# Kernel tuning notes

Hardware: AMD Instinct MI355X
Metric: run time of the kernel (lower is better)

## Reference

```python
import jax, jax.numpy as jnp
import numpy as np
import math

B, S, D, H, L, F = 32, 512, 512, 8, 4, 1024
TD = 4 * D  # time embedding dim
DH = D // H
SCALE = 1.0 / math.sqrt(DH)


def _ln(x, g, b):
    m = jnp.mean(x, -1, keepdims=True)
    v = jnp.var(x, -1, keepdims=True)
    return (x - m) * jax.lax.rsqrt(v + 1e-5) * g + b


def setup_inputs() -> dict:
    key = jax.random.key(0)
    ks = jax.random.split(key, 12)
    w = lambda k, shp: jax.random.normal(k, shp, dtype=jnp.float32) * 0.02
    return {
        "x": jax.random.normal(ks[0], (B, S, D), dtype=jnp.float32),
        "time": jax.random.uniform(ks[1], (B,), dtype=jnp.float32) * 1000.0,
        "time_w1": w(ks[2], (TD, D)), "time_b1": jnp.zeros((TD,), jnp.float32),
        "time_w2": w(ks[3], (TD, TD)), "time_b2": jnp.zeros((TD,), jnp.float32),
        "Wq": w(ks[4], (L, D, D)), "bq": jnp.zeros((L, D), jnp.float32),
        "Wk": w(ks[5], (L, D, D)), "bk": jnp.zeros((L, D), jnp.float32),
        "Wv": w(ks[6], (L, D, D)), "bv": jnp.zeros((L, D), jnp.float32),
        "Wo": w(ks[7], (L, D, D)), "bo": jnp.zeros((L, D), jnp.float32),
        "attn_g": jnp.ones((L, D), jnp.float32), "attn_b": jnp.zeros((L, D), jnp.float32),
        "ffn_g": jnp.ones((L, D), jnp.float32), "ffn_b": jnp.zeros((L, D), jnp.float32),
        "W1": w(ks[8], (L, 2 * F, D)), "b1": jnp.zeros((L, 2 * F), jnp.float32),
        "W2": w(ks[9], (L, D, F)), "b2": jnp.zeros((L, D), jnp.float32),
        "Wt": w(ks[10], (L, 4 * F, TD)), "bt": jnp.zeros((L, 4 * F), jnp.float32),
        "head_g": jnp.ones((D,), jnp.float32), "head_b": jnp.zeros((D,), jnp.float32),
        "Wh": w(ks[11], (D, D)), "bh": jnp.zeros((D,), jnp.float32),
    }


def _forward(x, time, time_w1, time_b1, time_w2, time_b2,
             Wq, bq, Wk, bk, Wv, bv, Wo, bo,
             attn_g, attn_b, ffn_g, ffn_b,
             W1, b1, W2, b2, Wt, bt,
             head_g, head_b, Wh, bh):
    Bsz = x.shape[0]
    # --- sinusoidal time embedding + time MLP ---
    half = D // 2
    freqs = jnp.exp(jnp.arange(half, dtype=jnp.float32) * (-math.log(10000.0) / (half - 1)))
    e = time[:, None] * freqs[None, :]
    temb = jnp.concatenate([jnp.sin(e), jnp.cos(e)], axis=-1)  # [B, D]
    temb = jax.nn.gelu(temb @ time_w1.T + time_b1, approximate=False) @ time_w2.T + time_b2  # [B, 4D]
    for i in range(L):
        # attention (prenorm; block 0 skips the norm since first_prenormalization=False)
        h = x if i == 0 else _ln(x, attn_g[i], attn_b[i])
        q = (h @ Wq[i].T + bq[i]).reshape(Bsz, S, H, DH)
        k = (h @ Wk[i].T + bk[i]).reshape(Bsz, S, H, DH)
        v = (h @ Wv[i].T + bv[i]).reshape(Bsz, S, H, DH)
        logits = jnp.einsum('bqhd,bkhd->bhqk', q, k) * SCALE
        probs = jax.nn.softmax(logits, axis=-1)
        o = jnp.einsum('bhqk,bkhd->bqhd', probs, v).reshape(Bsz, S, D)
        x = x + (o @ Wo[i].T + bo[i])
        # FFN with FiLM time conditioning and ReGLU activation
        h = _ln(x, ffn_g[i], ffn_b[i])
        h1 = h @ W1[i].T + b1[i]  # [B, S, 2F]
        tm = jax.nn.silu(temb) @ Wt[i].T + bt[i]  # [B, 4F]
        scale, shift = jnp.split(tm[:, None, :], 2, axis=-1)  # each [B, 1, 2F]
        h1 = h1 * (scale + 1.0) + shift
        a, g = jnp.split(h1, 2, axis=-1)  # ReGLU: a * relu(g)
        x = x + ((a * jax.nn.relu(g)) @ W2[i].T + b2[i])
    # head: last token -> LayerNorm -> ReLU -> Linear
    z = _ln(x[:, -1], head_g, head_b)
    return jax.nn.relu(z) @ Wh.T + bh


def reference(x, time, time_w1, time_b1, time_w2, time_b2,
              Wq, bq, Wk, bk, Wv, bv, Wo, bo,
              attn_g, attn_b, ffn_g, ffn_b,
              W1, b1, W2, b2, Wt, bt,
              head_g, head_b, Wh, bh):
    return _forward(x, time, time_w1, time_b1, time_w2, time_b2,
                    Wq, bq, Wk, bk, Wv, bv, Wo, bo,
                    attn_g, attn_b, ffn_g, ffn_b,
                    W1, b1, W2, b2, Wt, bt,
                    head_g, head_b, Wh, bh)
```

## Files before the change

### kernel.cpp

```cpp
#include <hip/hip_runtime.h>
#include <math.h>

typedef __bf16 bf16_t;
typedef __bf16 bf16x8 __attribute__((ext_vector_type(8)));
typedef float f32x4 __attribute__((ext_vector_type(4)));

__device__ __forceinline__ void gload_lds16(const void* g, void* l) {
    __builtin_amdgcn_global_load_lds(
        (const __attribute__((address_space(1))) void*)g,
        (__attribute__((address_space(3))) void*)l, 16, 0, 0);
}

__global__ void k_f2b(const float* __restrict__ in, bf16_t* __restrict__ out, int n8) {
    int idx = blockIdx.x * 256 + threadIdx.x;
    if (idx >= n8) return;
    const float* p = in + (size_t)idx * 8;
    bf16x8 r;
#pragma unroll
    for (int j = 0; j < 8; j++) r[j] = (bf16_t)p[j];
    *(bf16x8*)(out + (size_t)idx * 8) = r;
}

__global__ void k_f2b_s(const float* __restrict__ in, bf16_t* __restrict__ out,
                        int seg8, int dstride8) {
    int idx = blockIdx.x * 256 + threadIdx.x;
    int seg = idx / seg8, rem = idx - seg * seg8;
    const float* p = in + (size_t)idx * 8;
    bf16x8 r;
#pragma unroll
    for (int j = 0; j < 8; j++) r[j] = (bf16_t)p[j];
    *(bf16x8*)(out + ((size_t)seg * dstride8 + rem) * 8) = r;
}

__global__ void k_time_embed(const float* __restrict__ time, float* __restrict__ temb0) {
    int b = blockIdx.x;
    int j = threadIdx.x;
    float f = __expf((float)j * -0.036118981458730134f);
    float e = time[b] * f;
    temb0[(size_t)b * 512 + j] = sinf(e);
    temb0[(size_t)b * 512 + 256 + j] = cosf(e);
}

template<bool DO_NORM, bool IN32>
__global__ void k_ln(const void* __restrict__ xp, const float* __restrict__ g,
                     const float* __restrict__ b, bf16_t* __restrict__ out) {
    int row = blockIdx.x * 4 + (threadIdx.x >> 6);
    int lane = threadIdx.x & 63;
    float vals[8];
    if (IN32) {
        const float* xr = (const float*)xp + (size_t)row * 512 + lane * 8;
        float4 v0 = *(const float4*)xr;
        float4 v1 = *(const float4*)(xr + 4);
        vals[0] = v0.x; vals[1] = v0.y; vals[2] = v0.z; vals[3] = v0.w;
        vals[4] = v1.x; vals[5] = v1.y; vals[6] = v1.z; vals[7] = v1.w;
    } else {
        bf16x8 xv = *(const bf16x8*)((const bf16_t*)xp + (size_t)row * 512 + lane * 8);
#pragma unroll
        for (int j = 0; j < 8; j++) vals[j] = (float)xv[j];
    }
    bf16x8 r;
    if (DO_NORM) {
        float s = 0.f, sq = 0.f;
#pragma unroll
        for (int j = 0; j < 8; j++) { s += vals[j]; sq += vals[j] * vals[j]; }
#pragma unroll
        for (int m = 1; m < 64; m <<= 1) { s += __shfl_xor(s, m, 64); sq += __shfl_xor(sq, m, 64); }
        float mean = s * (1.0f / 512.0f);
        float var = sq * (1.0f / 512.0f) - mean * mean;
        float rstd = rsqrtf(var + 1e-5f);
        float4 g0 = *(const float4*)(g + lane * 8);
        float4 g1 = *(const float4*)(g + lane * 8 + 4);
        float4 b0 = *(const float4*)(b + lane * 8);
        float4 b1 = *(const float4*)(b + lane * 8 + 4);
        float gs[8] = {g0.x, g0.y, g0.z, g0.w, g1.x, g1.y, g1.z, g1.w};
        float bs[8] = {b0.x, b0.y, b0.z, b0.w, b1.x, b1.y, b1.z, b1.w};
#pragma unroll
        for (int j = 0; j < 8; j++) r[j] = (bf16_t)((vals[j] - mean) * rstd * gs[j] + bs[j]);
    } else {
#pragma unroll
        for (int j = 0; j < 8; j++) r[j] = (bf16_t)vals[j];
    }
    *(bf16x8*)(out + (size_t)row * 512 + lane * 8) = r;
}

__global__ void k_head_prep(const bf16_t* __restrict__ x, const float* __restrict__ g,
                            const float* __restrict__ b, float* __restrict__ z) {
    int row = blockIdx.x * 4 + (threadIdx.x >> 6);
    int lane = threadIdx.x & 63;
    bf16x8 xv = *(const bf16x8*)(x + ((size_t)row * 512 + 511) * 512 + lane * 8);
    float vals[8];
#pragma unroll
    for (int j = 0; j < 8; j++) vals[j] = (float)xv[j];
    float s = 0.f, sq = 0.f;
#pragma unroll
    for (int j = 0; j < 8; j++) { s += vals[j]; sq += vals[j] * vals[j]; }
#pragma unroll
    for (int m = 1; m < 64; m <<= 1) { s += __shfl_xor(s, m, 64); sq += __shfl_xor(sq, m, 64); }
    float mean = s * (1.0f / 512.0f);
    float var = sq * (1.0f / 512.0f) - mean * mean;
    float rstd = rsqrtf(var + 1e-5f);
    float o[8];
#pragma unroll
    for (int j = 0; j < 8; j++) {
        float gv = g[lane * 8 + j], bv = b[lane * 8 + j];
        o[j] = fmaxf((vals[j] - mean) * rstd * gv + bv, 0.0f);
    }
    float* zr = z + (size_t)row * 512 + lane * 8;
    *(float4*)zr = make_float4(o[0], o[1], o[2], o[3]);
    *(float4*)(zr + 4) = make_float4(o[4], o[5], o[6], o[7]);
}

template<int ACT, int K, bool OUTB>
__global__ __launch_bounds__(256, 2)
void k_gemm_tm(const float* __restrict__ A, const float* __restrict__ W,
               const float* __restrict__ bias, void* __restrict__ outp, int N) {
    __shared__ float Asm[32][516];
    const int t = threadIdx.x;
    const int kq = t & 7, rw = (t >> 3) & 7, bh = t >> 6;
    const int n0 = blockIdx.x * 32;
    float acc[4][8] = {};
    for (int k0 = 0; k0 < K; k0 += 512) {
        __syncthreads();
#pragma unroll
        for (int i = 0; i < 16; i++) {
            int fid = t + i * 256;
            int row = fid >> 7, cc = (fid & 127) << 2;
            *(float4*)&Asm[row][cc] = *(const float4*)&A[(size_t)row * K + k0 + cc];
        }
        __syncthreads();
#pragma unroll 4
        for (int j = 0; j < 16; j++) {
            int kk = kq * 4 + j * 32;
            float4 w4[4];
#pragma unroll
            for (int r = 0; r < 4; r++)
                w4[r] = *(const float4*)&W[(size_t)(n0 + rw + r * 8) * K + k0 + kk];
#pragma unroll
            for (int b = 0; b < 8; b++) {
                float4 a4 = *(const float4*)&Asm[bh * 8 + b][kk];
#pragma unroll
                for (int r = 0; r < 4; r++)
                    acc[r][b] += a4.x * w4[r].x + a4.y * w4[r].y + a4.z * w4[r].z + a4.w * w4[r].w;
            }
        }
    }
#pragma unroll
    for (int m = 1; m < 8; m <<= 1)
#pragma unroll
        for (int r = 0; r < 4; r++)
#pragma unroll
            for (int b = 0; b < 8; b++)
                acc[r][b] += __shfl_xor(acc[r][b], m, 64);
    if (kq == 0) {
#pragma unroll
        for (int r = 0; r < 4; r++) {
            int n = n0 + rw + r * 8;
            float bv = bias[n];
#pragma unroll
            for (int b = 0; b < 8; b++) {
                float v = acc[r][b] + bv;
                if (ACT == 1) v = 0.5f * v * (1.0f + erff(v * 0.70710678118654752f));
                if (ACT == 2) v = v / (1.0f + __expf(-v));
                if (OUTB) ((bf16_t*)outp)[(size_t)(bh * 8 + b) * N + n] = (bf16_t)v;
                else      ((float*)outp)[(size_t)(bh * 8 + b) * N + n] = v;
            }
        }
    }
}

__global__ void k_fill_tmt(const float* __restrict__ bt, float* __restrict__ tm_t) {
    int i = blockIdx.x * 256 + threadIdx.x;
    tm_t[i] = bt[i >> 5];
}

__global__ __launch_bounds__(256, 4)
void k_gemm_wt(const float* __restrict__ Wt, const bf16_t* __restrict__ t2s_b,
               float* __restrict__ tm_t) {
    __shared__ __align__(16) bf16_t Abuf[64 * 64];
    __shared__ __align__(16) bf16_t Bbuf[32 * 64];
    const int tid = threadIdx.x;
    const int m0 = blockIdx.x * 64;
    const int k0 = blockIdx.y * 512;
    const int lane = tid & 63, wave = tid >> 6;
    const int arow = tid >> 2, aseg = tid & 3;
    const int brow = tid >> 3, bseg = tid & 7;
    const int aswz = (arow & 7) << 4;
    const char* Bg = (const char*)t2s_b + (size_t)brow * 4096 + ((bseg * 16) ^ ((brow & 7) << 4));
    char* BbL = (char*)Bbuf + tid * 16;
    const float* Ar0 = Wt + (size_t)(m0 + arow) * 2048 + k0 + aseg * 16;
    f32x4 acc[2] = {};
    for (int kk0 = 0; kk0 < 512; kk0 += 64) {
        float4 a4[4];
#pragma unroll
        for (int i = 0; i < 4; i++) a4[i] = *(const float4*)(Ar0 + kk0 + i * 4);
        __syncthreads();
        gload_lds16(Bg + (size_t)(k0 + kk0) * 2, BbL);
        bf16x8 c0, c1;
#pragma unroll
        for (int i = 0; i < 4; i++) {
            const float* af = (const float*)&a4[i];
#pragma unroll
            for (int j = 0; j < 4; j++) {
                if (i < 2) c0[i * 4 + j] = (bf16_t)af[j];
                else       c1[(i - 2) * 4 + j] = (bf16_t)af[j];
            }
        }
        int base = arow * 128 + aseg * 32;
        *(bf16x8*)((char*)Abuf + (base ^ aswz)) = c0;
        *(bf16x8*)((char*)Abuf + ((base + 16) ^ aswz)) = c1;
        __syncthreads();
#pragma unroll
        for (int kk = 0; kk < 2; kk++) {
            int ar = wave * 16 + (lane & 15);
            bf16x8 af = *(const bf16x8*)((const char*)Abuf + ar * 128 +
                        ((kk * 64 + (lane >> 4) * 16) ^ ((ar & 7) << 4)));
#pragma unroll
            for (int j = 0; j < 2; j++) {
                int br = j * 16 + (lane & 15);
                bf16x8 bfr = *(const bf16x8*)((const char*)Bbuf + br * 128 +
                             ((kk * 64 + (lane >> 4) * 16) ^ ((br & 7) << 4)));
                acc[j] = __builtin_amdgcn_mfma_f32_16x16x32_bf16(af, bfr, acc[j], 0, 0, 0);
            }
        }
    }
#pragma unroll
    for (int j = 0; j < 2; j++)
#pragma unroll
        for (int r = 0; r < 4; r++) {
            int mrow = m0 + wave * 16 + (lane >> 4) * 4 + r;
            atomicAdd(&tm_t[(size_t)mrow * 32 + j * 16 + (lane & 15)], acc[j][r]);
        }
}

enum { EPI_QKV = 0, EPI_RESID = 1, EPI_FILMGLU = 2 };

template<int EPI, int K, int NBY, int BM, bool RS32>
__global__ __launch_bounds__(BM * 2, 4)
void k_gemm_bt(const bf16_t* __restrict__ A, const bf16_t* __restrict__ W,
               const float* __restrict__ bias, const float* __restrict__ bias2,
               const float* __restrict__ bias3,
               void* __restrict__ out0, const void* __restrict__ rsp, void* __restrict__ out2,
               const float* __restrict__ tm) {
    constexpr int T   = BM * 2;
    constexpr int RPR = BM / 4;
    constexpr int BR  = 512 / BM;
    __shared__ __align__(16) bf16_t Abuf[BM * 64];
    __shared__ __align__(16) bf16_t Bbuf[128 * 64];
    const int tid = threadIdx.x;
    const int cpx = gridDim.x >> 3;
    const int wg = (blockIdx.x & 7) * cpx + (blockIdx.x >> 3);
    const int bx = wg / NBY;
    const int by = wg - bx * NBY;
    const int m0 = bx * BM;
    const int lane = tid & 63;
    const int wid = tid >> 6;
    const int wrM = (wid >> 1) * 64;
    const int wN  = wid & 1;
    const int wc  = wN * 64;

    const int srow = tid >> 3;
    const int goff = ((tid & 7) * 16) ^ ((srow & 7) << 4);
    const char* Ag = (const char*)A;
    const char* Wg = (const char*)W;
    char* AbL = (char*)Abuf + tid * 16;
    char* BbL = (char*)Bbuf + tid * 16;
    int growB[BR];
#pragma unroll
    for (int i = 0; i < BR; i++) {
        int r = srow + i * RPR;
        if (EPI == EPI_FILMGLU) {
            int half = (r >> 5) & 1;
            int base = by * 64 + (r >> 6) * 32 + (r & 31);
            growB[i] = half * 1024 + base;
        } else {
            growB[i] = by * 128 + r;
        }
    }

    f32x4 acc[4][4] = {};
    for (int k0 = 0; k0 < K * 2; k0 += 128) {
        __syncthreads();
#pragma unroll
        for (int i = 0; i < 4; i++)
            gload_lds16(Ag + (size_t)(m0 + srow + i * RPR) * (K * 2) + k0 + goff, AbL + i * (T * 16));
#pragma unroll
        for (int i = 0; i < BR; i++)
            gload_lds16(Wg + (size_t)growB[i] * (K * 2) + k0 + goff, BbL + i * (T * 16));
        __syncthreads();
#pragma unroll
        for (int kk = 0; kk < 2; kk++) {
            bf16x8 af[4], bfr[4];
#pragma unroll
            for (int i = 0; i < 4; i++) {
                int ar = wrM + i * 16 + (lane & 15);
                af[i] = *(const bf16x8*)((const char*)Abuf + ar * 128 +
                         ((kk * 64 + (lane >> 4) * 16) ^ ((ar & 7) << 4)));
                int br = wc + i * 16 + (lane & 15);
                bfr[i] = *(const bf16x8*)((const char*)Bbuf + br * 128 +
                         ((kk * 64 + (lane >> 4) * 16) ^ ((br & 7) << 4)));
            }
#pragma unroll
            for (int i = 0; i < 4; i++)
#pragma unroll
                for (int j = 0; j < 4; j++)
                    acc[i][j] = __builtin_amdgcn_mfma_f32_16x16x32_bf16(af[i], bfr[j], acc[i][j], 0, 0, 0);
        }
    }

    const int b = m0 >> 9;
    if (EPI == EPI_QKV) {
        const int which = by >> 2;
        bf16_t* op = (bf16_t*)(which == 0 ? out0 : which == 1 ? (void*)rsp : out2);
        const float* bp = which == 0 ? bias : which == 1 ? bias2 : bias3;
#pragma unroll
        for (int i = 0; i < 4; i++) {
#pragma unroll
            for (int r = 0; r < 4; r++) {
                int s = (m0 + wrM + i * 16 + (lane >> 4) * 4 + r) & 511;
#pragma unroll
                for (int j = 0; j < 4; j++) {
                    int c = (by & 3) * 128 + wc + j * 16 + (lane & 15);
                    float v = acc[i][j][r] + bp[c];
                    int h = c >> 6, dh = c & 63;
                    op[(((size_t)b * 8 + h) * 512 + s) * 64 + dh] = (bf16_t)v;
                }
            }
        }
    } else if (EPI == EPI_RESID) {
        bf16_t* op = (bf16_t*)out0;
#pragma unroll
        for (int i = 0; i < 4; i++) {
#pragma unroll
            for (int r = 0; r < 4; r++) {
                int row = m0 + wrM + i * 16 + (lane >> 4) * 4 + r;
#pragma unroll
                for (int j = 0; j < 4; j++) {
                    int col = by * 128 + wc + j * 16 + (lane & 15);
                    size_t idx = (size_t)row * 512 + col;
                    float rsv = RS32 ? ((const float*)rsp)[idx] : (float)((const bf16_t*)rsp)[idx];
                    op[idx] = (bf16_t)(rsv + acc[i][j][r] + bias[col]);
                }
            }
        }
    } else {
        bf16_t* op = (bf16_t*)out0;
#pragma unroll
        for (int i = 0; i < 4; i++) {
#pragma unroll
            for (int r = 0; r < 4; r++) {
                int row = m0 + wrM + i * 16 + (lane >> 4) * 4 + r;
#pragma unroll
                for (int jj = 0; jj < 2; jj++) {
                    int colA = by * 64 + wN * 32 + jj * 16 + (lane & 15);
                    float av = acc[i][jj][r] + bias[colA];
                    float gv = acc[i][jj + 2][r] + bias[1024 + colA];
                    float sa = tm[(size_t)colA * 32 + b];
                    float ha = tm[(size_t)(2048 + colA) * 32 + b];
                    float sg = tm[(size_t)(1024 + colA) * 32 + b];
                    float hg = tm[(size_t)(3072 + colA) * 32 + b];
                    av = av * (1.0f + sa) + ha;
                    gv = gv * (1.0f + sg) + hg;
                    op[(size_t)row * 1024 + colA] = (bf16_t)(av * fmaxf(gv, 0.0f));
                }
            }
        }
    }
}

__global__ __launch_bounds__(256, 2)
void k_attn(const bf16_t* __restrict__ q, const bf16_t* __restrict__ k,
            const bf16_t* __restrict__ v, bf16_t* __restrict__ o) {
    __shared__ bf16_t q_lds[64][72];
    __shared__ bf16_t k_lds[64][72];
    __shared__ bf16_t vt_lds[64 * 72];
    __shared__ bf16_t p_lds[64][72];
    const int tid = threadIdx.x;
    const int lane = tid & 63;
    const int wave = tid >> 6;
    const int cpx = gridDim.x >> 3;
    const int wg = ((int)blockIdx.x & 7) * cpx + ((int)blockIdx.x >> 3);
    const int bh = wg >> 3;
    const int qt = wg & 7;
    const bf16_t* qb = q + ((size_t)bh * 512 + qt * 64) * 64;
    const bf16_t* kb = k + (size_t)bh * 512 * 64;
    const bf16_t* vb = v + (size_t)bh * 512 * 64;
    const int sr = tid >> 2;
    const int sc = (tid & 3) * 16;
    {
        bf16x8 a0 = *(const bf16x8*)(qb + sr * 64 + sc);
        bf16x8 a1 = *(const bf16x8*)(qb + sr * 64 + sc + 8);
        bf16x8 ra, rb;
#pragma unroll
        for (int j = 0; j < 8; j++) {
            ra[j] = (bf16_t)((float)a0[j] * 0.125f);
            rb[j] = (bf16_t)((float)a1[j] * 0.125f);
        }
        *(bf16x8*)&q_lds[sr][sc] = ra;
        *(bf16x8*)&q_lds[sr][sc + 8] = rb;
    }
    bf16x8 kr0, kr1, vr0, vr1;
    {
        const bf16_t* ks = kb + (size_t)sr * 64 + sc;
        const bf16_t* vs = vb + (size_t)sr * 64 + sc;
        kr0 = *(const bf16x8*)ks; kr1 = *(const bf16x8*)(ks + 8);
        vr0 = *(const bf16x8*)vs; vr1 = *(const bf16x8*)(vs + 8);
    }
    float mrow[4], lrow[4];
    f32x4 oacc[4] = {};
#pragma unroll
    for (int r = 0; r < 4; r++) { mrow[r] = -1e30f; lrow[r] = 0.f; }
    const int swz0 = ((sc >> 3) & 7) << 4;
    const int swz1 = (((sc + 8) >> 3) & 7) << 4;
    for (int kt = 0; kt < 8; kt++) {
        __syncthreads();
        {
            *(bf16x8*)&k_lds[sr][sc] = kr0;
            *(bf16x8*)&k_lds[sr][sc + 8] = kr1;
            char* vbase = (char*)vt_lds;
            int so0 = (sr * 2) ^ swz0;
            int so1 = (sr * 2) ^ swz1;
#pragma unroll
            for (int j = 0; j < 8; j++) {
                *(bf16_t*)(vbase + (sc + j) * 144 + so0) = vr0[j];
                *(bf16_t*)(vbase + (sc + 8 + j) * 144 + so1) = vr1[j];
            }
        }
        __syncthreads();
        if (kt < 7) {
            const bf16_t* ks = kb + ((size_t)(kt + 1) * 64 + sr) * 64 + sc;
            const bf16_t* vs = vb + ((size_t)(kt + 1) * 64 + sr) * 64 + sc;
            kr0 = *(const bf16x8*)ks; kr1 = *(const bf16x8*)(ks + 8);
            vr0 = *(const bf16x8*)vs; vr1 = *(const bf16x8*)(vs + 8);
        }
        f32x4 sacc[4] = {};
#pragma unroll
        for (int kk = 0; kk < 2; kk++) {
            bf16x8 aq = *(const bf16x8*)&q_lds[wave * 16 + (lane & 15)][kk * 32 + (lane >> 4) * 8];
#pragma unroll
            for (int c = 0; c < 4; c++) {
                bf16x8 bk8 = *(const bf16x8*)&k_lds[c * 16 + (lane & 15)][kk * 32 + (lane >> 4) * 8];
                sacc[c] = __builtin_amdgcn_mfma_f32_16x16x32_bf16(aq, bk8, sacc[c], 0, 0, 0);
            }
        }
#pragma unroll
        for (int r = 0; r < 4; r++) {
            float mx = fmaxf(fmaxf(sacc[0][r], sacc[1][r]), fmaxf(sacc[2][r], sacc[3][r]));
#pragma unroll
            for (int m = 1; m < 16; m <<= 1) mx = fmaxf(mx, __shfl_xor(mx, m, 64));
            float newm = fmaxf(mrow[r], mx);
            float fsc = __expf(mrow[r] - newm);
            mrow[r] = newm;
            float p0 = __expf(sacc[0][r] - newm);
            float p1 = __expf(sacc[1][r] - newm);
            float p2 = __expf(sacc[2][r] - newm);
            float p3 = __expf(sacc[3][r] - newm);
            float ps = p0 + p1 + p2 + p3;
#pragma unroll
            for (int m = 1; m < 16; m <<= 1) ps += __shfl_xor(ps, m, 64);
            lrow[r] = lrow[r] * fsc + ps;
#pragma unroll
            for (int c = 0; c < 4; c++) oacc[c][r] *= fsc;
            int qrow = wave * 16 + (lane >> 4) * 4 + r;
            p_lds[qrow][(lane & 15)] = (bf16_t)p0;
            p_lds[qrow][16 + (lane & 15)] = (bf16_t)p1;
            p_lds[qrow][32 + (lane & 15)] = (bf16_t)p2;
            p_lds[qrow][48 + (lane & 15)] = (bf16_t)p3;
        }
#pragma unroll
        for (int kk = 0; kk < 2; kk++) {
            bf16x8 ap = *(const bf16x8*)&p_lds[wave * 16 + (lane & 15)][kk * 32 + (lane >> 4) * 8];
#pragma unroll
            for (int c = 0; c < 4; c++) {
                int d0 = c * 16 + (lane & 15);
                int xo = ((d0 >> 3) & 7) << 4;
                bf16x8 bv8 = *(const bf16x8*)((const char*)vt_lds + d0 * 144 +
                              ((kk * 64 + (lane >> 4) * 16) ^ xo));
                oacc[c] = __builtin_amdgcn_mfma_f32_16x16x32_bf16(ap, bv8, oacc[c], 0, 0, 0);
            }
        }
    }
    const int b = bh >> 3, h = bh & 7;
#pragma unroll
    for (int r = 0; r < 4; r++) {
        int s = qt * 64 + wave * 16 + (lane >> 4) * 4 + r;
        float inv = 1.0f / lrow[r];
#pragma unroll
        for (int c = 0; c < 4; c++) {
            o[((size_t)b * 512 + s) * 512 + h * 64 + c * 16 + (lane & 15)] = (bf16_t)(oacc[c][r] * inv);
        }
    }
}

extern "C" void kernel_launch(void* const* d_in, const int* in_sizes, int n_in,
                              void* d_out, int out_size, void* d_ws, size_t ws_size,
                              hipStream_t stream) {
    const float* x_in   = (const float*)d_in[0];
    const float* time_in= (const float*)d_in[1];
    const float* tw1    = (const float*)d_in[2];
    const float* tb1    = (const float*)d_in[3];
    const float* tw2    = (const float*)d_in[4];
    const float* tb2    = (const float*)d_in[5];
    const float* Wq     = (const float*)d_in[6];
    const float* bq     = (const float*)d_in[7];
    const float* Wk     = (const float*)d_in[8];
    const float* bk     = (const float*)d_in[9];
    const float* Wv     = (const float*)d_in[10];
    const float* bv     = (const float*)d_in[11];
    const float* Wo     = (const float*)d_in[12];
    const float* bo     = (const float*)d_in[13];
    const float* attn_g = (const float*)d_in[14];
    const float* attn_b = (const float*)d_in[15];
    const float* ffn_g  = (const float*)d_in[16];
    const float* ffn_b  = (const float*)d_in[17];
    const float* W1     = (const float*)d_in[18];
    const float* b1     = (const float*)d_in[19];
    const float* W2     = (const float*)d_in[20];
    const float* b2     = (const float*)d_in[21];
    const float* Wt     = (const float*)d_in[22];
    const float* bt     = (const float*)d_in[23];
    const float* head_g = (const float*)d_in[24];
    const float* head_b = (const float*)d_in[25];
    const float* Wh     = (const float*)d_in[26];
    const float* bh     = (const float*)d_in[27];

    size_t off = 0;
    auto alloc = [&](size_t bytes) {
        void* r = (char*)d_ws + off;
        off += (bytes + 255) & ~(size_t)255;
        return r;
    };
    bf16_t* wqkv_b = (bf16_t*)alloc((size_t)4 * 3 * 512 * 512 * 2);
    bf16_t* wo_b   = (bf16_t*)alloc((size_t)4 * 512 * 512 * 2);
    bf16_t* w1_b   = (bf16_t*)alloc((size_t)4 * 2048 * 512 * 2);
    bf16_t* w2_b   = (bf16_t*)alloc((size_t)4 * 512 * 1024 * 2);
    bf16_t* x_ws   = (bf16_t*)alloc((size_t)16384 * 512 * 2);
    bf16_t* h_b    = (bf16_t*)alloc((size_t)16384 * 512 * 2);
    bf16_t* q_b    = (bf16_t*)alloc((size_t)16384 * 512 * 2);
    bf16_t* k_b    = (bf16_t*)alloc((size_t)16384 * 512 * 2);
    bf16_t* v_b    = (bf16_t*)alloc((size_t)16384 * 512 * 2);
    bf16_t* o_b    = (bf16_t*)alloc((size_t)16384 * 512 * 2);
    bf16_t* act_b  = (bf16_t*)alloc((size_t)16384 * 1024 * 2);
    float*  temb0  = (float*)alloc((size_t)32 * 512 * 4);
    float*  t1     = (float*)alloc((size_t)32 * 2048 * 4);
    bf16_t* t2s_b  = (bf16_t*)alloc((size_t)32 * 2048 * 2);
    float*  tm_t   = (float*)alloc((size_t)16384 * 32 * 4);
    float*  z      = (float*)alloc((size_t)32 * 512 * 4);

    k_f2b_s<<<512, 256, 0, stream>>>(Wq, wqkv_b,          32768, 98304);
    k_f2b_s<<<512, 256, 0, stream>>>(Wk, wqkv_b + 262144, 32768, 98304);
    k_f2b_s<<<512, 256, 0, stream>>>(Wv, wqkv_b + 524288, 32768, 98304);
    k_f2b<<<512, 256, 0, stream>>>(Wo, wo_b, 131072);
    k_f2b<<<2048, 256, 0, stream>>>(W1, w1_b, 524288);
    k_f2b<<<1024, 256, 0, stream>>>(W2, w2_b, 262144);

    k_time_embed<<<32, 256, 0, stream>>>(time_in, temb0);
    k_gemm_tm<1, 512, false><<<64, 256, 0, stream>>>(temb0, tw1, tb1, t1, 2048);
    k_gemm_tm<2, 2048, true><<<64, 256, 0, stream>>>(t1, tw2, tb2, t2s_b, 2048);
    k_fill_tmt<<<2048, 256, 0, stream>>>(bt, tm_t);
    k_gemm_wt<<<dim3(256, 4), 256, 0, stream>>>(Wt, t2s_b, tm_t);

    for (int l = 0; l < 4; l++) {
        if (l == 0)
            k_ln<false, true><<<4096, 256, 0, stream>>>(x_in, nullptr, nullptr, h_b);
        else
            k_ln<true, false><<<4096, 256, 0, stream>>>(x_ws, attn_g + l * 512, attn_b + l * 512, h_b);

        k_gemm_bt<EPI_QKV, 512, 12, 256, false><<<768, 512, 0, stream>>>(
            h_b, wqkv_b + (size_t)l * 786432,
            bq + l * 512, bk + l * 512, bv + l * 512,
            q_b, k_b, v_b, nullptr);

        k_attn<<<2048, 256, 0, stream>>>(q_b, k_b, v_b, o_b);

        if (l == 0)
            k_gemm_bt<EPI_RESID, 512, 4, 128, true><<<512, 256, 0, stream>>>(
                o_b, wo_b + (size_t)l * 262144,
                bo + l * 512, nullptr, nullptr,
                x_ws, x_in, nullptr, nullptr);
        else
            k_gemm_bt<EPI_RESID, 512, 4, 128, false><<<512, 256, 0, stream>>>(
                o_b, wo_b + (size_t)l * 262144,
                bo + l * 512, nullptr, nullptr,
                x_ws, x_ws, nullptr, nullptr);

        k_ln<true, false><<<4096, 256, 0, stream>>>(x_ws, ffn_g + l * 512, ffn_b + l * 512, h_b);

        k_gemm_bt<EPI_FILMGLU, 512, 16, 256, false><<<1024, 512, 0, stream>>>(
            h_b, w1_b + (size_t)l * 1048576,
            b1 + l * 2048, nullptr, nullptr,
            act_b, nullptr, nullptr, tm_t + (size_t)l * 4096 * 32);

        k_gemm_bt<EPI_RESID, 1024, 4, 128, false><<<512, 256, 0, stream>>>(
            act_b, w2_b + (size_t)l * 524288,
            b2 + l * 512, nullptr, nullptr,
            x_ws, x_ws, nullptr, nullptr);
    }

    k_head_prep<<<8, 256, 0, stream>>>(x_ws, head_g, head_b, z);
    k_gemm_tm<0, 512, false><<<16, 256, 0, stream>>>(z, Wh, bh, (float*)d_out, 512);
}
```

Baseline: 1.092 ms.

## Process two query tiles per attention block, shrink GEMM tiles, reroute time-MLP GEMM

```diff
diff --git a/kernel.cpp b/kernel.cpp
--- a/kernel.cpp
+++ b/kernel.cpp
@@ -168,14 +168,22 @@
     }
 }
 
-__global__ void k_fill_tmt(const float* __restrict__ bt, float* __restrict__ tm_t) {
+__global__ void k_fill_tmt(const float* __restrict__ bt, float* __restrict__ dst) {
     int i = blockIdx.x * 256 + threadIdx.x;
-    tm_t[i] = bt[i >> 5];
+    dst[i] = bt[i >> 5];
+}
+
+__global__ void k_silu_t(const float* __restrict__ tmp, bf16_t* __restrict__ t2s_b) {
+    int i = blockIdx.x * 256 + threadIdx.x;
+    float v = tmp[i];
+    v = v / (1.0f + __expf(-v));
+    int n = i >> 5, b = i & 31;
+    t2s_b[(size_t)b * 2048 + n] = (bf16_t)v;
 }
 
 __global__ __launch_bounds__(256, 4)
-void k_gemm_wt(const float* __restrict__ Wt, const bf16_t* __restrict__ t2s_b,
-               float* __restrict__ tm_t) {
+void k_gemm_wt(const float* __restrict__ Wf, const bf16_t* __restrict__ Bb16,
+               float* __restrict__ dst) {
     __shared__ __align__(16) bf16_t Abuf[64 * 64];
     __shared__ __align__(16) bf16_t Bbuf[32 * 64];
     const int tid = threadIdx.x;
@@ -185,9 +193,9 @@
     const int arow = tid >> 2, aseg = tid & 3;
     const int brow = tid >> 3, bseg = tid & 7;
     const int aswz = (arow & 7) << 4;
-    const char* Bg = (const char*)t2s_b + (size_t)brow * 4096 + ((bseg * 16) ^ ((brow & 7) << 4));
+    const char* Bg = (const char*)Bb16 + (size_t)brow * 4096 + ((bseg * 16) ^ ((brow & 7) << 4));
     char* BbL = (char*)Bbuf + tid * 16;
-    const float* Ar0 = Wt + (size_t)(m0 + arow) * 2048 + k0 + aseg * 16;
+    const float* Ar0 = Wf + (size_t)(m0 + arow) * 2048 + k0 + aseg * 16;
     f32x4 acc[2] = {};
     for (int kk0 = 0; kk0 < 512; kk0 += 64) {
         float4 a4[4];
@@ -228,7 +236,7 @@
 #pragma unroll
         for (int r = 0; r < 4; r++) {
             int mrow = m0 + wave * 16 + (lane >> 4) * 4 + r;
-            atomicAdd(&tm_t[(size_t)mrow * 32 + j * 16 + (lane & 15)], acc[j][r]);
+            atomicAdd(&dst[(size_t)mrow * 32 + j * 16 + (lane & 15)], acc[j][r]);
         }
 }
 
@@ -370,7 +378,7 @@
 __global__ __launch_bounds__(256, 2)
 void k_attn(const bf16_t* __restrict__ q, const bf16_t* __restrict__ k,
             const bf16_t* __restrict__ v, bf16_t* __restrict__ o) {
-    __shared__ bf16_t q_lds[64][72];
+    __shared__ bf16_t q_lds[2][64][72];
     __shared__ bf16_t k_lds[64][72];
     __shared__ bf16_t vt_lds[64 * 72];
     __shared__ bf16_t p_lds[64][72];
@@ -379,14 +387,15 @@
     const int wave = tid >> 6;
     const int cpx = gridDim.x >> 3;
     const int wg = ((int)blockIdx.x & 7) * cpx + ((int)blockIdx.x >> 3);
-    const int bh = wg >> 3;
-    const int qt = wg & 7;
-    const bf16_t* qb = q + ((size_t)bh * 512 + qt * 64) * 64;
+    const int bh = wg >> 2;
+    const int qt2 = wg & 3;
     const bf16_t* kb = k + (size_t)bh * 512 * 64;
     const bf16_t* vb = v + (size_t)bh * 512 * 64;
     const int sr = tid >> 2;
     const int sc = (tid & 3) * 16;
-    {
+#pragma unroll
+    for (int qi = 0; qi < 2; qi++) {
+        const bf16_t* qb = q + ((size_t)bh * 512 + qt2 * 128 + qi * 64) * 64;
         bf16x8 a0 = *(const bf16x8*)(qb + sr * 64 + sc);
         bf16x8 a1 = *(const bf16x8*)(qb + sr * 64 + sc + 8);
         bf16x8 ra, rb;
@@ -395,8 +404,8 @@
             ra[j] = (bf16_t)((float)a0[j] * 0.125f);
             rb[j] = (bf16_t)((float)a1[j] * 0.125f);
         }
-        *(bf16x8*)&q_lds[sr][sc] = ra;
-        *(bf16x8*)&q_lds[sr][sc + 8] = rb;
+        *(bf16x8*)&q_lds[qi][sr][sc] = ra;
+        *(bf16x8*)&q_lds[qi][sr][sc + 8] = rb;
     }
     bf16x8 kr0, kr1, vr0, vr1;
     {
@@ -405,10 +414,12 @@
         kr0 = *(const bf16x8*)ks; kr1 = *(const bf16x8*)(ks + 8);
         vr0 = *(const bf16x8*)vs; vr1 = *(const bf16x8*)(vs + 8);
     }
-    float mrow[4], lrow[4];
-    f32x4 oacc[4] = {};
-#pragma unroll
-    for (int r = 0; r < 4; r++) { mrow[r] = -1e30f; lrow[r] = 0.f; }
+    float mrow[2][4], lrow[2][4];
+    f32x4 oacc[2][4] = {};
+#pragma unroll
+    for (int qi = 0; qi < 2; qi++)
+#pragma unroll
+        for (int r = 0; r < 4; r++) { mrow[qi][r] = -1e30f; lrow[qi][r] = 0.f; }
     const int swz0 = ((sc >> 3) & 7) << 4;
     const int swz1 = (((sc + 8) >> 3) & 7) << 4;
     for (int kt = 0; kt < 8; kt++) {
@@ -432,61 +443,67 @@
             kr0 = *(const bf16x8*)ks; kr1 = *(const bf16x8*)(ks + 8);
             vr0 = *(const bf16x8*)vs; vr1 = *(const bf16x8*)(vs + 8);
         }
-        f32x4 sacc[4] = {};
-#pragma unroll
-        for (int kk = 0; kk < 2; kk++) {
-            bf16x8 aq = *(const bf16x8*)&q_lds[wave * 16 + (lane & 15)][kk * 32 + (lane >> 4) * 8];
+#pragma unroll
+        for (int qi = 0; qi < 2; qi++) {
+            f32x4 sacc[4] = {};
+#pragma unroll
+            for (int kk = 0; kk < 2; kk++) {
+                bf16x8 aq = *(const bf16x8*)&q_lds[qi][wave * 16 + (lane & 15)][kk * 32 + (lane >> 4) * 8];
+#pragma unroll
+                for (int c = 0; c < 4; c++) {
+                    bf16x8 bk8 = *(const bf16x8*)&k_lds[c * 16 + (lane & 15)][kk * 32 + (lane >> 4) * 8];
+                    sacc[c] = __builtin_amdgcn_mfma_f32_16x16x32_bf16(aq, bk8, sacc[c], 0, 0, 0);
+                }
+            }
+#pragma unroll
+            for (int r = 0; r < 4; r++) {
+                float mx = fmaxf(fmaxf(sacc[0][r], sacc[1][r]), fmaxf(sacc[2][r], sacc[3][r]));
+#pragma unroll
+                for (int m = 1; m < 16; m <<= 1) mx = fmaxf(mx, __shfl_xor(mx, m, 64));
+                float newm = fmaxf(mrow[qi][r], mx);
+                float fsc = __expf(mrow[qi][r] - newm);
+                mrow[qi][r] = newm;
+                float p0 = __expf(sacc[0][r] - newm);
+                float p1 = __expf(sacc[1][r] - newm);
+                float p2 = __expf(sacc[2][r] - newm);
+                float p3 = __expf(sacc[3][r] - newm);
+                float ps = p0 + p1 + p2 + p3;
+#pragma unroll
+                for (int m = 1; m < 16; m <<= 1) ps += __shfl_xor(ps, m, 64);
+                lrow[qi][r] = lrow[qi][r] * fsc + ps;
+#pragma unroll
+                for (int c = 0; c < 4; c++) oacc[qi][c][r] *= fsc;
+                int qrow = wave * 16 + (lane >> 4) * 4 + r;
+                p_lds[qrow][(lane & 15)] = (bf16_t)p0;
+                p_lds[qrow][16 + (lane & 15)] = (bf16_t)p1;
+                p_lds[qrow][32 + (lane & 15)] = (bf16_t)p2;
+                p_lds[qrow][48 + (lane & 15)] = (bf16_t)p3;
+            }
+#pragma unroll
+            for (int kk = 0; kk < 2; kk++) {
+                bf16x8 ap = *(const bf16x8*)&p_lds[wave * 16 + (lane & 15)][kk * 32 + (lane >> 4) * 8];
+#pragma unroll
+                for (int c = 0; c < 4; c++) {
+                    int d0 = c * 16 + (lane & 15);
+                    int xo = ((d0 >> 3) & 7) << 4;
+                    bf16x8 bv8 = *(const bf16x8*)((const char*)vt_lds + d0 * 144 +
+                                  ((kk * 64 + (lane >> 4) * 16) ^ xo));
+                    oacc[qi][c] = __builtin_amdgcn_mfma_f32_16x16x32_bf16(ap, bv8, oacc[qi][c], 0, 0, 0);
+                }
+            }
+        }
+    }
+    const int b = bh >> 3, h = bh & 7;
+#pragma unroll
+    for (int qi = 0; qi < 2; qi++) {
+#pragma unroll
+        for (int r = 0; r < 4; r++) {
+            int s = qt2 * 128 + qi * 64 + wave * 16 + (lane >> 4) * 4 + r;
+            float inv = 1.0f / lrow[qi][r];
 #pragma unroll
             for (int c = 0; c < 4; c++) {
-                bf16x8 bk8 = *(const bf16x8*)&k_lds[c * 16 + (lane & 15)][kk * 32 + (lane >> 4) * 8];
-                sacc[c] = __builtin_amdgcn_mfma_f32_16x16x32_bf16(aq, bk8, sacc[c], 0, 0, 0);
-            }
-        }
-#pragma unroll
-        for (int r = 0; r < 4; r++) {
-            float mx = fmaxf(fmaxf(sacc[0][r], sacc[1][r]), fmaxf(sacc[2][r], sacc[3][r]));
-#pragma unroll
-            for (int m = 1; m < 16; m <<= 1) mx = fmaxf(mx, __shfl_xor(mx, m, 64));
-            float newm = fmaxf(mrow[r], mx);
-            float fsc = __expf(mrow[r] - newm);
-            mrow[r] = newm;
-            float p0 = __expf(sacc[0][r] - newm);
-            float p1 = __expf(sacc[1][r] - newm);
-            float p2 = __expf(sacc[2][r] - newm);
-            float p3 = __expf(sacc[3][r] - newm);
-            float ps = p0 + p1 + p2 + p3;
-#pragma unroll
-            for (int m = 1; m < 16; m <<= 1) ps += __shfl_xor(ps, m, 64);
-            lrow[r] = lrow[r] * fsc + ps;
-#pragma unroll
-            for (int c = 0; c < 4; c++) oacc[c][r] *= fsc;
-            int qrow = wave * 16 + (lane >> 4) * 4 + r;
-            p_lds[qrow][(lane & 15)] = (bf16_t)p0;
-            p_lds[qrow][16 + (lane & 15)] = (bf16_t)p1;
-            p_lds[qrow][32 + (lane & 15)] = (bf16_t)p2;
-            p_lds[qrow][48 + (lane & 15)] = (bf16_t)p3;
-        }
-#pragma unroll
-        for (int kk = 0; kk < 2; kk++) {
-            bf16x8 ap = *(const bf16x8*)&p_lds[wave * 16 + (lane & 15)][kk * 32 + (lane >> 4) * 8];
-#pragma unroll
-            for (int c = 0; c < 4; c++) {
-                int d0 = c * 16 + (lane & 15);
-                int xo = ((d0 >> 3) & 7) << 4;
-                bf16x8 bv8 = *(const bf16x8*)((const char*)vt_lds + d0 * 144 +
-                              ((kk * 64 + (lane >> 4) * 16) ^ xo));
-                oacc[c] = __builtin_amdgcn_mfma_f32_16x16x32_bf16(ap, bv8, oacc[c], 0, 0, 0);
-            }
-        }
-    }
-    const int b = bh >> 3, h = bh & 7;
-#pragma unroll
-    for (int r = 0; r < 4; r++) {
-        int s = qt * 64 + wave * 16 + (lane >> 4) * 4 + r;
-        float inv = 1.0f / lrow[r];
-#pragma unroll
-        for (int c = 0; c < 4; c++) {
-            o[((size_t)b * 512 + s) * 512 + h * 64 + c * 16 + (lane & 15)] = (bf16_t)(oacc[c][r] * inv);
+                o[((size_t)b * 512 + s) * 512 + h * 64 + c * 16 + (lane & 15)] = (bf16_t)(oacc[qi][c][r] * inv);
+            }
         }
     }
 }
@@ -541,7 +558,8 @@
     bf16_t* o_b    = (bf16_t*)alloc((size_t)16384 * 512 * 2);
     bf16_t* act_b  = (bf16_t*)alloc((size_t)16384 * 1024 * 2);
     float*  temb0  = (float*)alloc((size_t)32 * 512 * 4);
-    float*  t1     = (float*)alloc((size_t)32 * 2048 * 4);
+    bf16_t* t1_b   = (bf16_t*)alloc((size_t)32 * 2048 * 2);
+    float*  tmp2   = (float*)alloc((size_t)2048 * 32 * 4);
     bf16_t* t2s_b  = (bf16_t*)alloc((size_t)32 * 2048 * 2);
     float*  tm_t   = (float*)alloc((size_t)16384 * 32 * 4);
     float*  z      = (float*)alloc((size_t)32 * 512 * 4);
@@ -554,8 +572,10 @@
     k_f2b<<<1024, 256, 0, stream>>>(W2, w2_b, 262144);
 
     k_time_embed<<<32, 256, 0, stream>>>(time_in, temb0);
-    k_gemm_tm<1, 512, false><<<64, 256, 0, stream>>>(temb0, tw1, tb1, t1, 2048);
-    k_gemm_tm<2, 2048, true><<<64, 256, 0, stream>>>(t1, tw2, tb2, t2s_b, 2048);
+    k_gemm_tm<1, 512, true><<<64, 256, 0, stream>>>(temb0, tw1, tb1, t1_b, 2048);
+    k_fill_tmt<<<256, 256, 0, stream>>>(tb2, tmp2);
+    k_gemm_wt<<<dim3(32, 4), 256, 0, stream>>>(tw2, t1_b, tmp2);
+    k_silu_t<<<256, 256, 0, stream>>>(tmp2, t2s_b);
     k_fill_tmt<<<2048, 256, 0, stream>>>(bt, tm_t);
     k_gemm_wt<<<dim3(256, 4), 256, 0, stream>>>(Wt, t2s_b, tm_t);
 
@@ -565,12 +585,12 @@
         else
             k_ln<true, false><<<4096, 256, 0, stream>>>(x_ws, attn_g + l * 512, attn_b + l * 512, h_b);
 
-        k_gemm_bt<EPI_QKV, 512, 12, 256, false><<<768, 512, 0, stream>>>(
+        k_gemm_bt<EPI_QKV, 512, 12, 128, false><<<1536, 256, 0, stream>>>(
             h_b, wqkv_b + (size_t)l * 786432,
             bq + l * 512, bk + l * 512, bv + l * 512,
             q_b, k_b, v_b, nullptr);
 
-        k_attn<<<2048, 256, 0, stream>>>(q_b, k_b, v_b, o_b);
+        k_attn<<<1024, 256, 0, stream>>>(q_b, k_b, v_b, o_b);
 
         if (l == 0)
             k_gemm_bt<EPI_RESID, 512, 4, 128, true><<<512, 256, 0, stream>>>(
@@ -585,7 +605,7 @@
 
         k_ln<true, false><<<4096, 256, 0, stream>>>(x_ws, ffn_g + l * 512, ffn_b + l * 512, h_b);
 
-        k_gemm_bt<EPI_FILMGLU, 512, 16, 256, false><<<1024, 512, 0, stream>>>(
+        k_gemm_bt<EPI_FILMGLU, 512, 16, 128, false><<<2048, 256, 0, stream>>>(
             h_b, w1_b + (size_t)l * 1048576,
             b1 + l * 2048, nullptr, nullptr,
             act_b, nullptr, nullptr, tm_t + (size_t)l * 4096 * 32);
```

Result: no change. 1.075 ms (-1.6%).
